# Optimization experiments

Hardware: AMD Instinct MI355X
Metric: run time of the kernel (lower is better)

Reference implementation:

```python
import jax, jax.numpy as jnp
import numpy as np

B = 32
N = 1024  # half_size == num_delays == num_wavelength
DELTA_TAU = 1.5e-15
W_CENTER = 1.175e15  # center_frequency / 2
PULSE_THRESHOLD = 0.01
PENALTY = 10.0
REAL_W = 1.0; IMAG_W = 1.0; INT_W = 1.0; PHASE_W = 1.0; FROG_W = 1.0
MSE_WSUM = REAL_W + IMAG_W + INT_W + PHASE_W

# Hilbert mask exactly as in the torch source (even N branch): H[N//2+1:]=2, H[N//2]=1
_Hm = np.zeros(N, dtype=np.float32)
_Hm[N // 2 + 1:] = 2.0
_Hm[N // 2] = 1.0
HILBERT_MASK = jnp.asarray(_Hm)

# precomputed circular-shift gather indices: shifted[m, j] = x[(j - delay[m]) mod N]
_delays = np.arange(-(N // 2), N // 2)
SHIFT_IDX = jnp.asarray((np.arange(N)[None, :] - _delays[:, None]) % N)  # [N, N] int
SHIFT_FACTOR = jnp.exp(-1j * jnp.asarray(2.0 * W_CENTER * DELTA_TAU * _delays, dtype=jnp.float32)).astype(jnp.complex64)  # [N]


def hilbert(x):  # x: [N] real -> [N] complex analytical signal
    xf = jnp.fft.fft(x)
    return jnp.fft.ifft(xf * HILBERT_MASK)


def shg_mat(a):  # a: [N] complex -> [N, N] complex SHG matrix (vectorized createSHGmat)
    shifted = a[SHIFT_IDX]                                  # [N, N] all circular shifts
    rows = a[None, :] * shifted * SHIFT_FACTOR[None, :]     # elementwise complex multiply
    f = jnp.fft.fft(jnp.fft.fftshift(rows, axes=-1), axis=-1)  # one batched FFT
    return DELTA_TAU * jnp.fft.fftshift(f, axes=-1)


def _first_last(mask):  # mask: [B, N] bool -> per-sample first/last significant index with fallback
    any_m = jnp.any(mask, axis=1)
    first = jnp.where(any_m, jnp.argmax(mask, axis=1), 0)
    last = jnp.where(any_m, N - 1 - jnp.argmax(mask[:, ::-1], axis=1), N - 1)
    return first, last


def setup_inputs() -> dict:
    key = jax.random.key(0)
    k1, k2, k3 = jax.random.split(key, 3)
    prediction = jax.random.normal(k1, (B, N), dtype=jnp.float32)
    label = jax.random.normal(k2, (B, 2 * N), dtype=jnp.float32)
    shg_matrix = jax.random.uniform(k3, (B, 1, N, N), dtype=jnp.float32)
    return {"prediction": prediction, "label": label, "shg_matrix": shg_matrix}


def reference(prediction, label, shg_matrix):
    pa = jax.vmap(hilbert)(prediction)          # [B, N] complex64
    pr, pi = pa.real, pa.imag
    lr, li = label[:, :N], label[:, N:]
    l_int = lr ** 2 + li ** 2
    p_int = pr ** 2 + pi ** 2
    l_ph = jnp.arctan2(li, lr)
    p_ph = jnp.arctan2(pi, pr)

    # ---- FROG error ----
    shg_pred = jnp.abs(jax.vmap(shg_mat)(pa)) ** 2              # [B, N, N]
    shg_pred = shg_pred / jnp.max(shg_pred, axis=(1, 2), keepdims=True)  # normalizeSHGmatrix
    t_ref = shg_matrix[:, 0]                                    # [B, N, N]
    sum1 = jnp.sum(shg_pred * t_ref, axis=(1, 2))
    sum2 = jnp.sum(t_ref * t_ref, axis=(1, 2))
    mu = sum1 / sum2
    r = jnp.sum(shg_pred - mu[:, None, None] * t_ref, axis=(1, 2)) ** 2
    norm = (N * N) * jnp.max(shg_pred, axis=(1, 2)) ** 2
    frog = jnp.where(r == 0.0, 0.0, jnp.sqrt(r / norm))         # [B]

    # ---- weighted masked MSE ----
    fr, lr_idx = _first_last(jnp.abs(lr) > PULSE_THRESHOLD)
    fi, li_idx = _first_last(jnp.abs(li) > PULSE_THRESHOLD)
    first = jnp.minimum(fr, fi)
    last = jnp.maximum(lr_idx, li_idx)
    ar = jnp.arange(N)[None, :]
    in_range = (ar >= first[:, None]) & (ar < last[:, None])    # [first:last] slice semantics
    phase_mask = in_range.astype(jnp.float32)
    pulse_mask = jnp.where(in_range, PENALTY, 1.0)

    mse_real = jnp.mean((pr - lr) ** 2 * pulse_mask, axis=1) * REAL_W
    mse_imag = jnp.mean((pi - li) ** 2 * pulse_mask, axis=1) * IMAG_W
    mse_int = jnp.mean((p_int - l_int) ** 2 * pulse_mask, axis=1) * INT_W
    mse_ph = jnp.mean((p_ph - l_ph) ** 2 * phase_mask, axis=1) * PHASE_W
    mse = (mse_real + mse_imag + mse_int + mse_ph) / MSE_WSUM

    return jnp.mean(mse + FROG_W * frog)
```

## Files before the change

kernel.cpp:

```cpp
#include <hip/hip_runtime.h>
#include <math.h>

#define N 1024
#define BATCH 32
#define NT 256
#define ROWS 4
#define RSTRIDE 1092
#define P16(i) ((i) + ((i) >> 4))
#define PADC(i) ((i) + ((i) >> 5))

#define WSYNC() asm volatile("s_waitcnt lgkmcnt(0)" ::: "memory")

typedef float2 cf;
__device__ __forceinline__ cf cadd(cf a, cf b){ return make_float2(a.x+b.x, a.y+b.y); }
__device__ __forceinline__ cf csub(cf a, cf b){ return make_float2(a.x-b.x, a.y-b.y); }
__device__ __forceinline__ cf cmul(cf a, cf b){ return make_float2(a.x*b.x - a.y*b.y, a.x*b.y + a.y*b.x); }

__device__ __forceinline__ cf twiddle(float jn){
    float s = __builtin_amdgcn_sinf(jn);
    float c = __builtin_amdgcn_cosf(jn);
    return make_float2(c, -s);
}

__device__ __forceinline__ int rev10(int m){
    int r = (int)(__brev((unsigned)m) >> 22);
    return ((r & 0x155) << 1) | ((r >> 1) & 0x155);
}

__device__ __forceinline__ void bfly(cf x0, cf x1, cf x2, cf x3,
                                     cf& y0, cf& y1, cf& y2, cf& y3){
    cf A = cadd(x0,x2), Bs = cadd(x1,x3);
    cf C = csub(x0,x2), D = csub(x1,x3);
    cf Dmi = make_float2(D.y, -D.x);
    y0 = cadd(A,Bs); y1 = cadd(C,Dmi); y2 = csub(A,Bs); y3 = csub(C,Dmi);
}

__device__ __forceinline__ void dif4p(cf* w, int base, int q, cf w1, cf w2, cf w3){
    cf x0 = w[P16(base)], x1 = w[P16(base+q)], x2 = w[P16(base+2*q)], x3 = w[P16(base+3*q)];
    cf y0, y1, y2, y3; bfly(x0,x1,x2,x3,y0,y1,y2,y3);
    w[P16(base)]     = y0;
    w[P16(base+q)]   = cmul(y1,w1);
    w[P16(base+2*q)] = cmul(y2,w2);
    w[P16(base+3*q)] = cmul(y3,w3);
}

__device__ __forceinline__ void dif4h(cf* w, int base, int q, float jn){
    cf x0 = w[PADC(base)], x1 = w[PADC(base+q)], x2 = w[PADC(base+2*q)], x3 = w[PADC(base+3*q)];
    cf y0, y1, y2, y3; bfly(x0,x1,x2,x3,y0,y1,y2,y3);
    cf w1 = twiddle(jn), w2 = cmul(w1,w1), w3 = cmul(w2,w1);
    w[PADC(base)]     = y0;
    w[PADC(base+q)]   = cmul(y1,w1);
    w[PADC(base+2*q)] = cmul(y2,w2);
    w[PADC(base+3*q)] = cmul(y3,w3);
}
template<int LOG2N>
__device__ __forceinline__ void dif_stage(cf* w, int t){
    const int n = 1 << LOG2N, q = n >> 2;
    int j = t & (q - 1);
    int base = ((t >> (LOG2N - 2)) << LOG2N) + j;
    dif4h(w, base, q, (float)j * (1.0f / (float)n));
}
template<int LOG2N>
__device__ __forceinline__ void dit_stage(cf* w, int t){
    const int n = 1 << LOG2N, q = n >> 2;
    int j = t & (q - 1);
    int base = ((t >> (LOG2N - 2)) << LOG2N) + j;
    cf x0 = w[PADC(base)], x1 = w[PADC(base+q)], x2 = w[PADC(base+2*q)], x3 = w[PADC(base+3*q)];
    cf w1 = twiddle((float)j * (1.0f / (float)n));
    cf w2 = cmul(w1,w1), w3 = cmul(w2,w1);
    x1 = cmul(x1,w1); x2 = cmul(x2,w2); x3 = cmul(x3,w3);
    cf y0, y1, y2, y3; bfly(x0,x1,x2,x3,y0,y1,y2,y3);
    w[PADC(base)] = y0; w[PADC(base+q)] = y1; w[PADC(base+2*q)] = y2; w[PADC(base+3*q)] = y3;
}

__global__ __launch_bounds__(NT) void hilbert_k(const float* __restrict__ pred,
                                                const float* __restrict__ label,
                                                cf* __restrict__ a,
                                                cf* __restrict__ ca,
                                                float* __restrict__ mseJ) {
    __shared__ cf wk[1056];
    __shared__ float rbuf[4][4];
    __shared__ int ibuf[4][4];
    __shared__ int s_first, s_last;
    int t = threadIdx.x, b = blockIdx.x;
    for (int i = t; i < N; i += NT) wk[PADC(i)] = make_float2(pred[b * N + i], 0.f);
    __syncthreads();
    dif_stage<10>(wk, t); __syncthreads();
    dif_stage<8>(wk, t);  __syncthreads();
    dif_stage<6>(wk, t);  __syncthreads();
    dif_stage<4>(wk, t);  __syncthreads();
    dif_stage<2>(wk, t);  __syncthreads();
    for (int i = t; i < N; i += NT) {
        int k = rev10(i);
        float f = (k < 512) ? 0.f : ((k == 512) ? 1.f : 2.f);
        cf v = wk[PADC(i)];
        wk[PADC(i)] = make_float2(f * v.x, -f * v.y);
    }
    __syncthreads();
    dit_stage<2>(wk, t);  __syncthreads();
    dit_stage<4>(wk, t);  __syncthreads();
    dit_stage<6>(wk, t);  __syncthreads();
    dit_stage<8>(wk, t);  __syncthreads();
    dit_stage<10>(wk, t); __syncthreads();
    const float sc = 1.f / (float)N;
    for (int i = t; i < N; i += NT) {
        cf v = wk[PADC(i)];
        cf av = make_float2(v.x * sc, -v.y * sc);
        wk[PADC(i)] = av;
        a[b * N + i] = av;
        float p = (float)(3.525 * (double)(i - 512));
        float s_, c_;
        sincosf(p, &s_, &c_);
        ca[b * N + i] = make_float2(av.x * c_ + av.y * s_, av.y * c_ - av.x * s_);
    }
    __syncthreads();

    int w = t >> 6, lane = t & 63;
    int mnR = N, mxR = -1, mnI = N, mxI = -1;
    for (int n = t; n < N; n += NT) {
        float lr = label[b * 2 * N + n];
        float li = label[b * 2 * N + N + n];
        if (fabsf(lr) > 0.01f) { mnR = min(mnR, n); mxR = max(mxR, n); }
        if (fabsf(li) > 0.01f) { mnI = min(mnI, n); mxI = max(mxI, n); }
    }
    for (int o = 32; o > 0; o >>= 1) {
        mnR = min(mnR, __shfl_down(mnR, o));
        mxR = max(mxR, __shfl_down(mxR, o));
        mnI = min(mnI, __shfl_down(mnI, o));
        mxI = max(mxI, __shfl_down(mxI, o));
    }
    if (lane == 0) { ibuf[w][0] = mnR; ibuf[w][1] = mxR; ibuf[w][2] = mnI; ibuf[w][3] = mxI; }
    __syncthreads();
    if (t == 0) {
        int a0 = N, a1 = -1, a2 = N, a3 = -1;
        for (int i = 0; i < 4; ++i) {
            a0 = min(a0, ibuf[i][0]); a1 = max(a1, ibuf[i][1]);
            a2 = min(a2, ibuf[i][2]); a3 = max(a3, ibuf[i][3]);
        }
        int fr   = (a0 == N) ? 0 : a0;
        int lstR = (a1 < 0) ? (N - 1) : a1;
        int fi   = (a2 == N) ? 0 : a2;
        int lstI = (a3 < 0) ? (N - 1) : a3;
        s_first = min(fr, fi);
        s_last  = max(lstR, lstI);
    }
    __syncthreads();
    int first = s_first, last = s_last;

    float m_r = 0.f, m_i = 0.f, m_n = 0.f, m_p = 0.f;
    for (int n = t; n < N; n += NT) {
        cf p = wk[PADC(n)];
        float lr = label[b * 2 * N + n];
        float li = label[b * 2 * N + N + n];
        bool in = (n >= first) && (n < last);
        float pm  = in ? 10.f : 1.f;
        float phm = in ? 1.f : 0.f;
        float dr = p.x - lr, di = p.y - li;
        float dn = (p.x * p.x + p.y * p.y) - (lr * lr + li * li);
        float dp = atan2f(p.y, p.x) - atan2f(li, lr);
        m_r += dr * dr * pm;
        m_i += di * di * pm;
        m_n += dn * dn * pm;
        m_p += dp * dp * phm;
    }
    for (int o = 32; o > 0; o >>= 1) {
        m_r += __shfl_down(m_r, o);
        m_i += __shfl_down(m_i, o);
        m_n += __shfl_down(m_n, o);
        m_p += __shfl_down(m_p, o);
    }
    if (lane == 0) { rbuf[w][0] = m_r; rbuf[w][1] = m_i; rbuf[w][2] = m_n; rbuf[w][3] = m_p; }
    __syncthreads();
    if (t == 0) {
        float s = 0.f;
        for (int i = 0; i < 4; ++i) s += rbuf[i][0] + rbuf[i][1] + rbuf[i][2] + rbuf[i][3];
        mseJ[b] = s * (1.f / (float)N) * 0.25f;
    }
}

__global__ __launch_bounds__(NT) void shg_k(const cf* __restrict__ a,
                                            const cf* __restrict__ cag,
                                            const float* __restrict__ tref,
                                            float* __restrict__ Praw,
                                            float* __restrict__ Prt,
                                            float* __restrict__ Pmax,
                                            float* __restrict__ Pt,
                                            float* __restrict__ Ptt) {
    __shared__ cf wk[ROWS * RSTRIDE];
    __shared__ float rbuf[4][ROWS][5];
    int t = threadIdx.x, blk = blockIdx.x;
    int b = blk >> 8;
    int dg = (blk & 255) << 2;
    const cf* arow  = a   + b * N;
    const cf* carow = cag + b * N;

    {
        cf w1 = twiddle((float)t * (1.0f / 1024.0f));
        cf w2 = cmul(w1,w1), w3 = cmul(w2,w1);
        cf cav[4];
#pragma unroll
        for (int k = 0; k < 4; ++k) cav[k] = carow[(t + 256*k + 512) & 1023];
#pragma unroll
        for (int r = 0; r < ROWS; ++r) {
            int d = dg + r;
            cf x[4];
#pragma unroll
            for (int k = 0; k < 4; ++k)
                x[k] = cmul(cav[k], arow[(t + 256*k - d) & 1023]);
            cf y0, y1, y2, y3; bfly(x[0],x[1],x[2],x[3],y0,y1,y2,y3);
            cf* w = wk + r * RSTRIDE;
            w[P16(t)]     = y0;
            w[P16(t+256)] = cmul(y1,w1);
            w[P16(t+512)] = cmul(y2,w2);
            w[P16(t+768)] = cmul(y3,w3);
        }
    }
    __syncthreads();
    {
        int j = t & 63;
        int base = ((t >> 6) << 8) + j;
        cf w1 = twiddle((float)j * (1.0f / 256.0f));
        cf w2 = cmul(w1,w1), w3 = cmul(w2,w1);
#pragma unroll
        for (int r = 0; r < ROWS; ++r) dif4p(wk + r * RSTRIDE, base, 64, w1, w2, w3);
    }
    WSYNC();
    {
        int j = t & 15;
        int base = ((t >> 4) << 6) + j;
        cf w1 = twiddle((float)j * (1.0f / 64.0f));
        cf w2 = cmul(w1,w1), w3 = cmul(w2,w1);
#pragma unroll
        for (int r = 0; r < ROWS; ++r) dif4p(wk + r * RSTRIDE, base, 16, w1, w2, w3);
    }
    WSYNC();

    float sraw = 0.f, srt = 0.f, mx = 0.f, st = 0.f, stt = 0.f;
    {
        const cf W1 = { 0.923879533f, -0.382683432f};
        const cf W2 = { 0.707106781f, -0.707106781f};
        const cf W3 = { 0.382683432f, -0.923879533f};
        const cf W6 = {-0.707106781f, -0.707106781f};
        const cf W9 = {-0.923879533f,  0.382683432f};
        int r = t & 3;
        int g = ((t >> 6) << 4) + ((t >> 2) & 15);
        cf* w = wk + r * RSTRIDE;
        cf v[16];
        int base = 17 * g;
#pragma unroll
        for (int k = 0; k < 16; ++k) v[k] = w[base + k];
        cf o[16];
        bfly(v[0], v[4], v[8], v[12], o[0], o[4], o[8],  o[12]);
        { cf y0,y1,y2,y3; bfly(v[1],v[5],v[9], v[13],y0,y1,y2,y3);
          o[1]=y0; o[5]=cmul(y1,W1); o[9]=cmul(y2,W2); o[13]=cmul(y3,W3); }
        { cf y0,y1,y2,y3; bfly(v[2],v[6],v[10],v[14],y0,y1,y2,y3);
          o[2]=y0; o[6]=cmul(y1,W2); o[10]=make_float2(y2.y,-y2.x); o[14]=cmul(y3,W6); }
        { cf y0,y1,y2,y3; bfly(v[3],v[7],v[11],v[15],y0,y1,y2,y3);
          o[3]=y0; o[7]=cmul(y1,W3); o[11]=cmul(y2,W6); o[15]=cmul(y3,W9); }
        int bd = b * N + dg + r;
        const float* trow = tref + ((size_t)bd << 10);
        int kb = ((g & 3) << 4) | (g & 12) | (g >> 4);
#pragma unroll
        for (int u = 0; u < 4; ++u) {
            cf y0, y1, y2, y3;
            bfly(o[4*u], o[4*u+1], o[4*u+2], o[4*u+3], y0, y1, y2, y3);
            cf ys[4] = {y0, y1, y2, y3};
#pragma unroll
            for (int m = 0; m < 4; ++m) {
                float m2 = ys[m].x * ys[m].x + ys[m].y * ys[m].y;
                float tv = trow[(((m + 2) & 3) << 8) | (u << 6) | kb];
                sraw += m2;
                srt += m2 * tv;
                mx = fmaxf(mx, m2);
                st += tv;
                stt += tv * tv;
            }
        }
    }
    for (int o = 32; o >= 4; o >>= 1) {
        sraw += __shfl_down(sraw, o);
        srt  += __shfl_down(srt, o);
        mx    = fmaxf(mx, __shfl_down(mx, o));
        st   += __shfl_down(st, o);
        stt  += __shfl_down(stt, o);
    }
    {
        int lane = t & 63, wv = t >> 6;
        if (lane < 4) {
            rbuf[wv][lane][0] = sraw; rbuf[wv][lane][1] = srt; rbuf[wv][lane][2] = mx;
            rbuf[wv][lane][3] = st;   rbuf[wv][lane][4] = stt;
        }
    }
    __syncthreads();
    if (t < ROWS) {
        float a0 = 0.f, a1 = 0.f, a2 = 0.f, a3 = 0.f, a4 = 0.f;
        for (int i = 0; i < 4; ++i) {
            a0 += rbuf[i][t][0]; a1 += rbuf[i][t][1]; a2 = fmaxf(a2, rbuf[i][t][2]);
            a3 += rbuf[i][t][3]; a4 += rbuf[i][t][4];
        }
        int bd = b * N + dg + t;
        Praw[bd] = a0; Prt[bd] = a1; Pmax[bd] = a2; Pt[bd] = a3; Ptt[bd] = a4;
    }
}

__global__ __launch_bounds__(NT) void loss_k(const float* __restrict__ Praw,
                                             const float* __restrict__ Prt,
                                             const float* __restrict__ Pmax,
                                             const float* __restrict__ Pt,
                                             const float* __restrict__ Ptt,
                                             const float* __restrict__ mseJ,
                                             float* __restrict__ out) {
    __shared__ float rbuf[4][8];
    int tid = threadIdx.x, b = blockIdx.x;
    int w = tid >> 6, lane = tid & 63;
    float sr = 0.f, srt = 0.f, mx = 0.f, st = 0.f, stt = 0.f;
    for (int i = tid; i < N; i += NT) {
        int idx = b * N + i;
        sr += Praw[idx]; srt += Prt[idx]; mx = fmaxf(mx, Pmax[idx]);
        st += Pt[idx];   stt += Ptt[idx];
    }
    for (int o = 32; o > 0; o >>= 1) {
        sr  += __shfl_down(sr, o);
        srt += __shfl_down(srt, o);
        mx   = fmaxf(mx, __shfl_down(mx, o));
        st  += __shfl_down(st, o);
        stt += __shfl_down(stt, o);
    }
    if (lane == 0) {
        rbuf[w][0] = sr; rbuf[w][1] = srt; rbuf[w][2] = mx;
        rbuf[w][3] = st; rbuf[w][4] = stt;
    }
    __syncthreads();
    if (tid == 0) {
        float A0 = 0.f, A1 = 0.f, A2 = 0.f, A3 = 0.f, A4 = 0.f;
        for (int i = 0; i < 4; ++i) {
            A0 += rbuf[i][0]; A1 += rbuf[i][1]; A2 = fmaxf(A2, rbuf[i][2]);
            A3 += rbuf[i][3]; A4 += rbuf[i][4];
        }
        float mu = (A1 / A2) / A4;
        float diff = A0 / A2 - mu * A3;
        float frog = fabsf(diff) * (1.f / (float)N);
        atomicAdd(out, (mseJ[b] + frog) * (1.f / (float)BATCH));
    }
}

extern "C" void kernel_launch(void* const* d_in, const int* in_sizes, int n_in,
                              void* d_out, int out_size, void* d_ws, size_t ws_size,
                              hipStream_t stream) {
    (void)in_sizes; (void)n_in; (void)out_size; (void)ws_size;
    const float* pred  = (const float*)d_in[0];
    const float* label = (const float*)d_in[1];
    const float* shg   = (const float*)d_in[2];
    float* out = (float*)d_out;

    char* ws = (char*)d_ws;
    cf* a   = (cf*)ws;
    cf* ca  = a + (size_t)BATCH * N;
    float* mseJ = (float*)(ca + (size_t)BATCH * N);
    float* P = mseJ + BATCH;
    float* Praw = P;
    float* Prt  = P + (size_t)BATCH * N;
    float* Pmax = P + 2 * (size_t)BATCH * N;
    float* Pt   = P + 3 * (size_t)BATCH * N;
    float* Ptt  = P + 4 * (size_t)BATCH * N;

    hipMemsetAsync(d_out, 0, sizeof(float), stream);
    hilbert_k<<<BATCH, NT, 0, stream>>>(pred, label, a, ca, mseJ);
    shg_k<<<BATCH * 256, NT, 0, stream>>>(a, ca, shg, Praw, Prt, Pmax, Pt, Ptt);
    loss_k<<<BATCH, NT, 0, stream>>>(Praw, Prt, Pmax, Pt, Ptt, mseJ, out);
}
```

Before: 231.7 us.

## Double SHG block threads and give each final-stage row its own wavefront

```diff
diff --git a/kernel.cpp b/kernel.cpp
--- a/kernel.cpp
+++ b/kernel.cpp
@@ -3,7 +3,7 @@
 
 #define N 1024
 #define BATCH 32
-#define NT 256
+#define NT 512
 #define ROWS 4
 #define RSTRIDE 1092
 #define P16(i) ((i) + ((i) >> 4))
@@ -73,24 +73,24 @@
     w[PADC(base)] = y0; w[PADC(base+q)] = y1; w[PADC(base+2*q)] = y2; w[PADC(base+3*q)] = y3;
 }
 
-__global__ __launch_bounds__(NT) void hilbert_k(const float* __restrict__ pred,
-                                                const float* __restrict__ label,
-                                                cf* __restrict__ a,
-                                                cf* __restrict__ ca,
-                                                float* __restrict__ mseJ) {
+__global__ __launch_bounds__(256) void hilbert_k(const float* __restrict__ pred,
+                                                 const float* __restrict__ label,
+                                                 cf* __restrict__ a,
+                                                 cf* __restrict__ ca,
+                                                 float* __restrict__ mseJ) {
     __shared__ cf wk[1056];
     __shared__ float rbuf[4][4];
     __shared__ int ibuf[4][4];
     __shared__ int s_first, s_last;
     int t = threadIdx.x, b = blockIdx.x;
-    for (int i = t; i < N; i += NT) wk[PADC(i)] = make_float2(pred[b * N + i], 0.f);
+    for (int i = t; i < N; i += 256) wk[PADC(i)] = make_float2(pred[b * N + i], 0.f);
     __syncthreads();
     dif_stage<10>(wk, t); __syncthreads();
     dif_stage<8>(wk, t);  __syncthreads();
     dif_stage<6>(wk, t);  __syncthreads();
     dif_stage<4>(wk, t);  __syncthreads();
     dif_stage<2>(wk, t);  __syncthreads();
-    for (int i = t; i < N; i += NT) {
+    for (int i = t; i < N; i += 256) {
         int k = rev10(i);
         float f = (k < 512) ? 0.f : ((k == 512) ? 1.f : 2.f);
         cf v = wk[PADC(i)];
@@ -103,7 +103,7 @@
     dit_stage<8>(wk, t);  __syncthreads();
     dit_stage<10>(wk, t); __syncthreads();
     const float sc = 1.f / (float)N;
-    for (int i = t; i < N; i += NT) {
+    for (int i = t; i < N; i += 256) {
         cf v = wk[PADC(i)];
         cf av = make_float2(v.x * sc, -v.y * sc);
         wk[PADC(i)] = av;
@@ -117,7 +117,7 @@
 
     int w = t >> 6, lane = t & 63;
     int mnR = N, mxR = -1, mnI = N, mxI = -1;
-    for (int n = t; n < N; n += NT) {
+    for (int n = t; n < N; n += 256) {
         float lr = label[b * 2 * N + n];
         float li = label[b * 2 * N + N + n];
         if (fabsf(lr) > 0.01f) { mnR = min(mnR, n); mxR = max(mxR, n); }
@@ -148,7 +148,7 @@
     int first = s_first, last = s_last;
 
     float m_r = 0.f, m_i = 0.f, m_n = 0.f, m_p = 0.f;
-    for (int n = t; n < N; n += NT) {
+    for (int n = t; n < N; n += 256) {
         cf p = wk[PADC(n)];
         float lr = label[b * 2 * N + n];
         float li = label[b * 2 * N + N + n];
@@ -178,72 +178,72 @@
     }
 }
 
-__global__ __launch_bounds__(NT) void shg_k(const cf* __restrict__ a,
-                                            const cf* __restrict__ cag,
-                                            const float* __restrict__ tref,
-                                            float* __restrict__ Praw,
-                                            float* __restrict__ Prt,
-                                            float* __restrict__ Pmax,
-                                            float* __restrict__ Pt,
-                                            float* __restrict__ Ptt) {
+__global__ __launch_bounds__(NT, 8) void shg_k(const cf* __restrict__ a,
+                                               const cf* __restrict__ cag,
+                                               const float* __restrict__ tref,
+                                               float* __restrict__ Praw,
+                                               float* __restrict__ Prt,
+                                               float* __restrict__ Pmax,
+                                               float* __restrict__ Pt,
+                                               float* __restrict__ Ptt) {
     __shared__ cf wk[ROWS * RSTRIDE];
-    __shared__ float rbuf[4][ROWS][5];
     int t = threadIdx.x, blk = blockIdx.x;
     int b = blk >> 8;
     int dg = (blk & 255) << 2;
     const cf* arow  = a   + b * N;
     const cf* carow = cag + b * N;
+    int bt = t & 255, rg = t >> 8;
 
     {
-        cf w1 = twiddle((float)t * (1.0f / 1024.0f));
+        cf w1 = twiddle((float)bt * (1.0f / 1024.0f));
         cf w2 = cmul(w1,w1), w3 = cmul(w2,w1);
         cf cav[4];
 #pragma unroll
-        for (int k = 0; k < 4; ++k) cav[k] = carow[(t + 256*k + 512) & 1023];
-#pragma unroll
-        for (int r = 0; r < ROWS; ++r) {
+        for (int k = 0; k < 4; ++k) cav[k] = carow[(bt + 256*k + 512) & 1023];
+#pragma unroll
+        for (int rr = 0; rr < 2; ++rr) {
+            int r = rg * 2 + rr;
             int d = dg + r;
             cf x[4];
 #pragma unroll
             for (int k = 0; k < 4; ++k)
-                x[k] = cmul(cav[k], arow[(t + 256*k - d) & 1023]);
+                x[k] = cmul(cav[k], arow[(bt + 256*k - d) & 1023]);
             cf y0, y1, y2, y3; bfly(x[0],x[1],x[2],x[3],y0,y1,y2,y3);
             cf* w = wk + r * RSTRIDE;
-            w[P16(t)]     = y0;
-            w[P16(t+256)] = cmul(y1,w1);
-            w[P16(t+512)] = cmul(y2,w2);
-            w[P16(t+768)] = cmul(y3,w3);
+            w[P16(bt)]     = y0;
+            w[P16(bt+256)] = cmul(y1,w1);
+            w[P16(bt+512)] = cmul(y2,w2);
+            w[P16(bt+768)] = cmul(y3,w3);
         }
     }
     __syncthreads();
     {
-        int j = t & 63;
-        int base = ((t >> 6) << 8) + j;
+        int j = bt & 63;
+        int base = ((bt >> 6) << 8) + j;
         cf w1 = twiddle((float)j * (1.0f / 256.0f));
         cf w2 = cmul(w1,w1), w3 = cmul(w2,w1);
 #pragma unroll
-        for (int r = 0; r < ROWS; ++r) dif4p(wk + r * RSTRIDE, base, 64, w1, w2, w3);
+        for (int rr = 0; rr < 2; ++rr) dif4p(wk + (rg*2+rr) * RSTRIDE, base, 64, w1, w2, w3);
     }
     WSYNC();
     {
-        int j = t & 15;
-        int base = ((t >> 4) << 6) + j;
+        int j = bt & 15;
+        int base = ((bt >> 4) << 6) + j;
         cf w1 = twiddle((float)j * (1.0f / 64.0f));
         cf w2 = cmul(w1,w1), w3 = cmul(w2,w1);
 #pragma unroll
-        for (int r = 0; r < ROWS; ++r) dif4p(wk + r * RSTRIDE, base, 16, w1, w2, w3);
-    }
-    WSYNC();
-
-    float sraw = 0.f, srt = 0.f, mx = 0.f, st = 0.f, stt = 0.f;
-    {
+        for (int rr = 0; rr < 2; ++rr) dif4p(wk + (rg*2+rr) * RSTRIDE, base, 16, w1, w2, w3);
+    }
+    __syncthreads();
+
+    if (t < 256) {
         const cf W1 = { 0.923879533f, -0.382683432f};
         const cf W2 = { 0.707106781f, -0.707106781f};
         const cf W3 = { 0.382683432f, -0.923879533f};
         const cf W6 = {-0.707106781f, -0.707106781f};
         const cf W9 = {-0.923879533f,  0.382683432f};
-        int r = t & 3;
-        int g = ((t >> 6) << 4) + ((t >> 2) & 15);
+        int r = t >> 6;
+        int g = t & 63;
         cf* w = wk + r * RSTRIDE;
         cf v[16];
         int base = 17 * g;
@@ -257,6 +257,8 @@
           o[2]=y0; o[6]=cmul(y1,W2); o[10]=make_float2(y2.y,-y2.x); o[14]=cmul(y3,W6); }
         { cf y0,y1,y2,y3; bfly(v[3],v[7],v[11],v[15],y0,y1,y2,y3);
           o[3]=y0; o[7]=cmul(y1,W3); o[11]=cmul(y2,W6); o[15]=cmul(y3,W9); }
+
+        float sraw = 0.f, srt = 0.f, mx = 0.f, st = 0.f, stt = 0.f;
         int bd = b * N + dg + r;
         const float* trow = tref + ((size_t)bd << 10);
         int kb = ((g & 3) << 4) | (g & 12) | (g >> 4);
@@ -276,45 +278,31 @@
                 stt += tv * tv;
             }
         }
-    }
-    for (int o = 32; o >= 4; o >>= 1) {
-        sraw += __shfl_down(sraw, o);
-        srt  += __shfl_down(srt, o);
-        mx    = fmaxf(mx, __shfl_down(mx, o));
-        st   += __shfl_down(st, o);
-        stt  += __shfl_down(stt, o);
-    }
-    {
-        int lane = t & 63, wv = t >> 6;
-        if (lane < 4) {
-            rbuf[wv][lane][0] = sraw; rbuf[wv][lane][1] = srt; rbuf[wv][lane][2] = mx;
-            rbuf[wv][lane][3] = st;   rbuf[wv][lane][4] = stt;
-        }
-    }
-    __syncthreads();
-    if (t < ROWS) {
-        float a0 = 0.f, a1 = 0.f, a2 = 0.f, a3 = 0.f, a4 = 0.f;
-        for (int i = 0; i < 4; ++i) {
-            a0 += rbuf[i][t][0]; a1 += rbuf[i][t][1]; a2 = fmaxf(a2, rbuf[i][t][2]);
-            a3 += rbuf[i][t][3]; a4 += rbuf[i][t][4];
-        }
-        int bd = b * N + dg + t;
-        Praw[bd] = a0; Prt[bd] = a1; Pmax[bd] = a2; Pt[bd] = a3; Ptt[bd] = a4;
-    }
-}
-
-__global__ __launch_bounds__(NT) void loss_k(const float* __restrict__ Praw,
-                                             const float* __restrict__ Prt,
-                                             const float* __restrict__ Pmax,
-                                             const float* __restrict__ Pt,
-                                             const float* __restrict__ Ptt,
-                                             const float* __restrict__ mseJ,
-                                             float* __restrict__ out) {
+        for (int o_ = 32; o_ > 0; o_ >>= 1) {
+            sraw += __shfl_down(sraw, o_);
+            srt  += __shfl_down(srt, o_);
+            mx    = fmaxf(mx, __shfl_down(mx, o_));
+            st   += __shfl_down(st, o_);
+            stt  += __shfl_down(stt, o_);
+        }
+        if ((t & 63) == 0) {
+            Praw[bd] = sraw; Prt[bd] = srt; Pmax[bd] = mx; Pt[bd] = st; Ptt[bd] = stt;
+        }
+    }
+}
+
+__global__ __launch_bounds__(256) void loss_k(const float* __restrict__ Praw,
+                                              const float* __restrict__ Prt,
+                                              const float* __restrict__ Pmax,
+                                              const float* __restrict__ Pt,
+                                              const float* __restrict__ Ptt,
+                                              const float* __restrict__ mseJ,
+                                              float* __restrict__ out) {
     __shared__ float rbuf[4][8];
     int tid = threadIdx.x, b = blockIdx.x;
     int w = tid >> 6, lane = tid & 63;
     float sr = 0.f, srt = 0.f, mx = 0.f, st = 0.f, stt = 0.f;
-    for (int i = tid; i < N; i += NT) {
+    for (int i = tid; i < N; i += 256) {
         int idx = b * N + i;
         sr += Praw[idx]; srt += Prt[idx]; mx = fmaxf(mx, Pmax[idx]);
         st += Pt[idx];   stt += Ptt[idx];
@@ -365,7 +353,7 @@
     float* Ptt  = P + 4 * (size_t)BATCH * N;
 
     hipMemsetAsync(d_out, 0, sizeof(float), stream);
-    hilbert_k<<<BATCH, NT, 0, stream>>>(pred, label, a, ca, mseJ);
+    hilbert_k<<<BATCH, 256, 0, stream>>>(pred, label, a, ca, mseJ);
     shg_k<<<BATCH * 256, NT, 0, stream>>>(a, ca, shg, Praw, Prt, Pmax, Pt, Ptt);
-    loss_k<<<BATCH, NT, 0, stream>>>(Praw, Prt, Pmax, Pt, Ptt, mseJ, out);
-}
+    loss_k<<<BATCH, 256, 0, stream>>>(Praw, Prt, Pmax, Pt, Ptt, mseJ, out);
+}
```

New measurement: 227.7 us. About the same (-1.7%).
